# Kernel optimization log

Hardware: AMD Instinct MI355X
Metric: run time of the kernel (lower is better)

The kernel has to match this reference:

```python
import jax, jax.numpy as jnp
import numpy as np

B, D, H, W = 8, 1024, 64, 64
NH = 16
HD = D // NH
EPS = 1e-5


def _pos_encoding(n, d, dtype):
    # standard 1D sinusoidal PE over flattened spatial positions, shape (n, d)
    pos = jnp.arange(n, dtype=jnp.float32)[:, None]
    i = jnp.arange(d)[None, :]
    rates = 1.0 / (10000.0 ** ((2 * (i // 2)).astype(jnp.float32) / d))
    ang = pos * rates
    pe = jnp.where(i % 2 == 0, jnp.sin(ang), jnp.cos(ang))
    return pe.astype(dtype)


def setup_inputs() -> dict:
    key = jax.random.key(0)
    ks = jax.random.split(key, 4)
    x = jax.random.normal(ks[0], (B, D, H, W), dtype=jnp.float32)
    context_token = jax.random.normal(ks[1], (B, 1, D), dtype=jnp.float32)
    Wqkv = jax.random.normal(ks[2], (3 * D, D), dtype=jnp.float32) * 0.02
    bqkv = jnp.zeros((3 * D,), dtype=jnp.float32)
    Wo = jax.random.normal(ks[3], (D, D), dtype=jnp.float32) * 0.02
    bo = jnp.zeros((D,), dtype=jnp.float32)
    gamma = jnp.ones((D,), dtype=jnp.float32)
    beta = jnp.zeros((D,), dtype=jnp.float32)
    return {"x": x, "context_token": context_token, "Wqkv": Wqkv, "bqkv": bqkv,
            "Wo": Wo, "bo": bo, "gamma": gamma, "beta": beta}


def reference(x, context_token, Wqkv, bqkv, Wo, bo, gamma, beta):
    b, d, h, w = x.shape
    hw = h * w
    # x_flat: (B, HW, D); add positional encoding
    x_flat = x.reshape(b, d, hw).transpose(0, 2, 1)
    x_flat = x_flat + _pos_encoding(hw, d, x.dtype)[None]
    xc = jnp.concatenate([context_token, x_flat], axis=1)  # (B, S, D), S = HW+1
    s = hw + 1

    qkv = xc @ Wqkv.T + bqkv                                 # (B, S, 3D)
    q, k, v = jnp.split(qkv, 3, axis=-1)
    k = k.reshape(b, s, NH, HD)
    v = v.reshape(b, s, NH, HD)
    scale = 1.0 / jnp.sqrt(jnp.asarray(HD, x.dtype))

    # Star attention: CLS query (row 0) attends to all keys
    q0 = q[:, 0].reshape(b, NH, HD)                          # (B, NH, HD)
    scores = jnp.einsum('bhd,bshd->bhs', q0, k) * scale      # (B, NH, S)
    probs = jax.nn.softmax(scores, axis=-1)
    cls_out = jnp.einsum('bhs,bshd->bhd', probs, v).reshape(b, d)

    # Token queries attend only to the CLS key -> softmax over 1 elem = 1 -> v_cls
    v_cls = v[:, 0].reshape(b, d)                            # (B, D)
    tok_out = jnp.broadcast_to(v_cls[:, None, :], (b, hw, d))

    attn = jnp.concatenate([cls_out[:, None, :], tok_out], axis=1)  # (B, S, D)
    attn = attn @ Wo.T + bo

    res = attn + xc
    mu = jnp.mean(res, axis=-1, keepdims=True)
    var = jnp.mean((res - mu) ** 2, axis=-1, keepdims=True)
    y = (res - mu) * jax.lax.rsqrt(var + EPS) * gamma + beta

    context_token_out = y[:, 0:1, :]
    feature_map_out = y[:, 1:, :].transpose(0, 2, 1).reshape(b, d, h, w)
    return feature_map_out, context_token_out
```

## Files before the change

### kernel.cpp

```cpp
#include <hip/hip_runtime.h>
#include <math.h>

#define B_ 8
#define D_ 1024
#define HW_ 4096
#define NH_ 16
#define EPS_ 1e-5f

#define PE_OFF   0u
#define Q0_OFF   4194304u
#define VCLS_OFF 4202496u
#define UT_OFF   4210688u
#define TB_OFF   4341760u
#define SC_OFF   4349952u
#define PT_OFF   4874240u
#define P0_OFF   5398528u
#define W_OFF    5398656u
#define CLS_OFF  5529728u
#define R0_OFF   5537920u

__global__ void k_pe(float* __restrict__ pe) {
    int idx = blockIdx.x * 256 + threadIdx.x;
    int p = idx & (HW_ - 1);
    int d = idx >> 12;
    float e = (float)(2 * (d >> 1));
    float rate = exp2f(e * (-13.287712379549449f / 1024.0f));
    float ang = (float)p * rate;
    float s, c;
    sincosf(ang, &s, &c);
    pe[idx] = (d & 1) ? c : s;
}

__global__ void k_qv(const float* __restrict__ Wqkv, const float* __restrict__ bqkv,
                     const float* __restrict__ ctx,
                     float* __restrict__ q0, float* __restrict__ vcls) {
    int wid  = (blockIdx.x * 256 + threadIdx.x) >> 6;
    int lane = threadIdx.x & 63;
    int isv  = wid >> 13;
    int r    = wid & 8191;
    int b = r >> 10, i = r & 1023;
    int row = isv ? (2 * D_ + i) : i;
    const float4* wr = (const float4*)(Wqkv + (size_t)row * D_);
    const float4* cb = (const float4*)(ctx + b * D_);
    float acc = 0.0f;
    for (int k = lane; k < 256; k += 64) {
        float4 a = wr[k], c = cb[k];
        acc += a.x * c.x + a.y * c.y + a.z * c.z + a.w * c.w;
    }
    for (int o = 32; o; o >>= 1) acc += __shfl_down(acc, o);
    if (lane == 0) {
        float v = acc + bqkv[row];
        if (isv) vcls[b * D_ + i] = v; else q0[b * D_ + i] = v;
    }
}

__global__ void k_u_tb(const float* __restrict__ Wqkv,
                       const float* __restrict__ Wo, const float* __restrict__ bo,
                       const float* __restrict__ q0, const float* __restrict__ vcls,
                       float* __restrict__ u_t, float* __restrict__ t_b) {
    if (blockIdx.x < 128) {
        int b = blockIdx.x >> 4, h = blockIdx.x & 15;
        int t = threadIdx.x;
        float a0 = 0, a1 = 0, a2 = 0, a3 = 0;
        const float* q0h = q0 + b * D_ + h * 64;
        for (int j = 0; j < 64; ++j) {
            float qj = q0h[j];
            const float* wr = Wqkv + (size_t)(D_ + h * 64 + j) * D_;
            a0 += qj * wr[t];
            a1 += qj * wr[t + 256];
            a2 += qj * wr[t + 512];
            a3 += qj * wr[t + 768];
        }
        float* ub = u_t + (size_t)(b * D_) * NH_ + h;
        ub[(size_t)t * 16]          = 0.125f * a0;
        ub[(size_t)(t + 256) * 16]  = 0.125f * a1;
        ub[(size_t)(t + 512) * 16]  = 0.125f * a2;
        ub[(size_t)(t + 768) * 16]  = 0.125f * a3;
    } else {
        int wid  = (blockIdx.x - 128) * 4 + (threadIdx.x >> 6);
        int lane = threadIdx.x & 63;
        int b = wid >> 10, i = wid & 1023;
        const float4* wr = (const float4*)(Wo + (size_t)i * D_);
        const float4* vb = (const float4*)(vcls + b * D_);
        float acc = 0.0f;
        for (int k = lane; k < 256; k += 64) {
            float4 a = wr[k], c = vb[k];
            acc += a.x * c.x + a.y * c.y + a.z * c.z + a.w * c.w;
        }
        for (int o = 32; o; o >>= 1) acc += __shfl_down(acc, o);
        if (lane == 0) t_b[b * D_ + i] = acc + bo[i];
    }
}

__global__ __launch_bounds__(512) void k_main(
        const float* __restrict__ x, const float* __restrict__ pe,
        const float* __restrict__ u_t, const float* __restrict__ t_b,
        const float* __restrict__ gamma, const float* __restrict__ beta,
        float* __restrict__ scores, float* __restrict__ out) {
    int wave = threadIdx.x >> 6, lane = threadIdx.x & 63;
    int b = blockIdx.y;
    int p = blockIdx.x * 64 + lane;
    const float* xb = x + (size_t)b * D_ * HW_;
    const float* tb = t_b + b * D_;
    float acc[16];
    #pragma unroll
    for (int h = 0; h < 16; ++h) acc[h] = 0.0f;
    float sum = 0.0f, sumsq = 0.0f;
    int d0 = wave * 128;
    for (int d = d0; d < d0 + 128; ++d) {
        float xv = xb[(size_t)d * HW_ + p];
        float pv = pe[(size_t)d * HW_ + p];
        float xc = xv + pv;
        float resv = xc + tb[d];
        sum += resv;
        sumsq += resv * resv;
        const float* up = u_t + (size_t)(b * D_ + d) * 16;
        #pragma unroll
        for (int h = 0; h < 16; ++h) acc[h] += up[h] * xc;
    }
    __shared__ float red[8][18][64];
    #pragma unroll
    for (int h = 0; h < 16; ++h) red[wave][h][lane] = acc[h];
    red[wave][16][lane] = sum;
    red[wave][17][lane] = sumsq;
    __syncthreads();
    for (int id = threadIdx.x; id < 1024; id += 512) {
        int h = id >> 6, l = id & 63;
        float s = 0.0f;
        #pragma unroll
        for (int w2 = 0; w2 < 8; ++w2) s += red[w2][h][l];
        scores[(size_t)(b * 16 + h) * HW_ + blockIdx.x * 64 + l] = s;
    }
    if (threadIdx.x < 64) {
        int l = threadIdx.x;
        float S = 0.0f, SQ = 0.0f;
        #pragma unroll
        for (int w2 = 0; w2 < 8; ++w2) { S += red[w2][16][l]; SQ += red[w2][17][l]; }
        float mu = S * (1.0f / D_);
        float var = SQ * (1.0f / D_) - mu * mu;
        red[0][16][l] = mu;
        red[0][17][l] = rsqrtf(var + EPS_);
    }
    __syncthreads();
    float mu = red[0][16][lane], rstd = red[0][17][lane];
    float* ob = out + (size_t)b * D_ * HW_;
    for (int d = d0; d < d0 + 128; ++d) {
        float resv = xb[(size_t)d * HW_ + p] + pe[(size_t)d * HW_ + p] + tb[d];
        ob[(size_t)d * HW_ + p] = (resv - mu) * rstd * gamma[d] + beta[d];
    }
}

__global__ void k_softmax(const float* __restrict__ scores, const float* __restrict__ u_t,
                          const float* __restrict__ ctx,
                          float* __restrict__ probs_tok, float* __restrict__ probs0) {
    int b = blockIdx.x >> 4, h = blockIdx.x & 15;
    int t = threadIdx.x;
    __shared__ float lds[256];
    float part = 0.0f;
    for (int d = t; d < D_; d += 256)
        part += u_t[(size_t)(b * D_ + d) * 16 + h] * ctx[b * D_ + d];
    lds[t] = part; __syncthreads();
    for (int o = 128; o; o >>= 1) { if (t < o) lds[t] += lds[t + o]; __syncthreads(); }
    float s0 = lds[0];
    __syncthreads();
    const float4* sr = (const float4*)(scores + (size_t)(b * 16 + h) * HW_);
    float4 v[4];
    float m = s0;
    #pragma unroll
    for (int k = 0; k < 4; ++k) {
        v[k] = sr[t + 256 * k];
        m = fmaxf(m, fmaxf(fmaxf(v[k].x, v[k].y), fmaxf(v[k].z, v[k].w)));
    }
    lds[t] = m; __syncthreads();
    for (int o = 128; o; o >>= 1) { if (t < o) lds[t] = fmaxf(lds[t], lds[t + o]); __syncthreads(); }
    m = lds[0];
    __syncthreads();
    float zs = 0.0f;
    #pragma unroll
    for (int k = 0; k < 4; ++k) {
        v[k].x = expf(v[k].x - m); v[k].y = expf(v[k].y - m);
        v[k].z = expf(v[k].z - m); v[k].w = expf(v[k].w - m);
        zs += v[k].x + v[k].y + v[k].z + v[k].w;
    }
    float e0 = expf(s0 - m);
    lds[t] = zs; __syncthreads();
    for (int o = 128; o; o >>= 1) { if (t < o) lds[t] += lds[t + o]; __syncthreads(); }
    float inv = 1.0f / (lds[0] + e0);
    float4* pr = (float4*)(probs_tok + (size_t)(b * 16 + h) * HW_);
    #pragma unroll
    for (int k = 0; k < 4; ++k) {
        float4 o4 = v[k];
        o4.x *= inv; o4.y *= inv; o4.z *= inv; o4.w *= inv;
        pr[t + 256 * k] = o4;
    }
    if (t == 0) probs0[b * 16 + h] = e0 * inv;
}

__global__ __launch_bounds__(512) void k_wacc(
        const float* __restrict__ x, const float* __restrict__ pe,
        const float* __restrict__ probs_tok, const float* __restrict__ probs0,
        const float* __restrict__ ctx, float* __restrict__ w) {
    int wave = threadIdx.x >> 6, lane = threadIdx.x & 63;
    int b = blockIdx.y;
    int d0 = blockIdx.x * 32 + wave * 4;
    const float* xb = x + (size_t)b * D_ * HW_;
    const float* pb = probs_tok + (size_t)b * 16 * HW_;
    float acc[4][16];
    #pragma unroll
    for (int r = 0; r < 4; ++r)
        #pragma unroll
        for (int h = 0; h < 16; ++h) acc[r][h] = 0.0f;
    for (int it = 0; it < 64; ++it) {
        int p = it * 64 + lane;
        float xv[4];
        #pragma unroll
        for (int r = 0; r < 4; ++r)
            xv[r] = xb[(size_t)(d0 + r) * HW_ + p] + pe[(size_t)(d0 + r) * HW_ + p];
        #pragma unroll
        for (int h = 0; h < 16; ++h) {
            float prv = pb[(size_t)h * HW_ + p];
            #pragma unroll
            for (int r = 0; r < 4; ++r) acc[r][h] += prv * xv[r];
        }
    }
    #pragma unroll
    for (int r = 0; r < 4; ++r)
        #pragma unroll
        for (int h = 0; h < 16; ++h) {
            float v = acc[r][h];
            for (int o = 32; o; o >>= 1) v += __shfl_down(v, o);
            acc[r][h] = v;
        }
    if (lane == 0) {
        #pragma unroll
        for (int h = 0; h < 16; ++h) {
            float p0 = probs0[b * 16 + h];
            #pragma unroll
            for (int r = 0; r < 4; ++r)
                w[(size_t)(b * 16 + h) * D_ + d0 + r] = acc[r][h] + p0 * ctx[b * D_ + d0 + r];
        }
    }
}

__global__ void k_cls(const float* __restrict__ Wqkv, const float* __restrict__ bqkv,
                      const float* __restrict__ w, float* __restrict__ cls) {
    int wid  = (blockIdx.x * 256 + threadIdx.x) >> 6;
    int lane = threadIdx.x & 63;
    int b = wid >> 10, i = wid & 1023, h = i >> 6;
    const float4* wr = (const float4*)(Wqkv + (size_t)(2 * D_ + i) * D_);
    const float4* wb = (const float4*)(w + (size_t)(b * 16 + h) * D_);
    float acc = 0.0f;
    for (int k = lane; k < 256; k += 64) {
        float4 a = wr[k], c = wb[k];
        acc += a.x * c.x + a.y * c.y + a.z * c.z + a.w * c.w;
    }
    for (int o = 32; o; o >>= 1) acc += __shfl_down(acc, o);
    if (lane == 0) cls[b * D_ + i] = acc + bqkv[2 * D_ + i];
}

__global__ void k_attn0(const float* __restrict__ Wo, const float* __restrict__ bo,
                        const float* __restrict__ cls, const float* __restrict__ ctx,
                        float* __restrict__ res0) {
    int wid  = (blockIdx.x * 256 + threadIdx.x) >> 6;
    int lane = threadIdx.x & 63;
    int b = wid >> 10, i = wid & 1023;
    const float4* wr = (const float4*)(Wo + (size_t)i * D_);
    const float4* cb = (const float4*)(cls + b * D_);
    float acc = 0.0f;
    for (int k = lane; k < 256; k += 64) {
        float4 a = wr[k], c = cb[k];
        acc += a.x * c.x + a.y * c.y + a.z * c.z + a.w * c.w;
    }
    for (int o = 32; o; o >>= 1) acc += __shfl_down(acc, o);
    if (lane == 0) res0[b * D_ + i] = acc + bo[i] + ctx[b * D_ + i];
}

__global__ void k_ln0(const float* __restrict__ res0, const float* __restrict__ gamma,
                      const float* __restrict__ beta, float* __restrict__ out) {
    int b = blockIdx.x, t = threadIdx.x;
    __shared__ float lds[512];
    float v[4];
    float s = 0.0f, sq = 0.0f;
    #pragma unroll
    for (int k = 0; k < 4; ++k) {
        v[k] = res0[b * D_ + t + 256 * k];
        s += v[k]; sq += v[k] * v[k];
    }
    lds[t] = s; lds[256 + t] = sq; __syncthreads();
    for (int o = 128; o; o >>= 1) {
        if (t < o) { lds[t] += lds[t + o]; lds[256 + t] += lds[256 + t + o]; }
        __syncthreads();
    }
    float mu = lds[0] * (1.0f / D_);
    float var = lds[256] * (1.0f / D_) - mu * mu;
    float rstd = rsqrtf(var + EPS_);
    #pragma unroll
    for (int k = 0; k < 4; ++k) {
        int i = t + 256 * k;
        out[(size_t)B_ * D_ * HW_ + b * D_ + i] = (v[k] - mu) * rstd * gamma[i] + beta[i];
    }
}

extern "C" void kernel_launch(void* const* d_in, const int* in_sizes, int n_in,
                              void* d_out, int out_size, void* d_ws, size_t ws_size,
                              hipStream_t stream) {
    const float* x     = (const float*)d_in[0];
    const float* ctx   = (const float*)d_in[1];
    const float* Wqkv  = (const float*)d_in[2];
    const float* bqkv  = (const float*)d_in[3];
    const float* Wo    = (const float*)d_in[4];
    const float* bo    = (const float*)d_in[5];
    const float* gamma = (const float*)d_in[6];
    const float* beta  = (const float*)d_in[7];
    float* out = (float*)d_out;
    float* ws  = (float*)d_ws;

    float* pe    = ws + PE_OFF;
    float* q0    = ws + Q0_OFF;
    float* vcls  = ws + VCLS_OFF;
    float* u_t   = ws + UT_OFF;
    float* t_b   = ws + TB_OFF;
    float* sc    = ws + SC_OFF;
    float* pt    = ws + PT_OFF;
    float* p0    = ws + P0_OFF;
    float* w     = ws + W_OFF;
    float* cls   = ws + CLS_OFF;
    float* r0    = ws + R0_OFF;

    k_pe<<<dim3(16384), dim3(256), 0, stream>>>(pe);
    k_qv<<<dim3(4096), dim3(256), 0, stream>>>(Wqkv, bqkv, ctx, q0, vcls);
    k_u_tb<<<dim3(2176), dim3(256), 0, stream>>>(Wqkv, Wo, bo, q0, vcls, u_t, t_b);
    k_main<<<dim3(64, 8), dim3(512), 0, stream>>>(x, pe, u_t, t_b, gamma, beta, sc, out);
    k_softmax<<<dim3(128), dim3(256), 0, stream>>>(sc, u_t, ctx, pt, p0);
    k_wacc<<<dim3(32, 8), dim3(512), 0, stream>>>(x, pe, pt, p0, ctx, w);
    k_cls<<<dim3(2048), dim3(256), 0, stream>>>(Wqkv, bqkv, w, cls);
    k_attn0<<<dim3(2048), dim3(256), 0, stream>>>(Wo, bo, cls, ctx, r0);
    k_ln0<<<dim3(8), dim3(256), 0, stream>>>(r0, gamma, beta, out);
}
```

Baseline: 495.0 us.

## Fuse LayerNorm output write into weighted-accumulation pass to drop one x read

```diff
diff --git a/kernel.cpp b/kernel.cpp
--- a/kernel.cpp
+++ b/kernel.cpp
@@ -8,27 +8,29 @@
 #define EPS_ 1e-5f
 
 #define PE_OFF   0u
-#define Q0_OFF   4194304u
-#define VCLS_OFF 4202496u
-#define UT_OFF   4210688u
-#define TB_OFF   4341760u
-#define SC_OFF   4349952u
-#define PT_OFF   4874240u
-#define P0_OFF   5398528u
-#define W_OFF    5398656u
-#define CLS_OFF  5529728u
-#define R0_OFF   5537920u
+#define UT_OFF   4194304u
+#define TB_OFF   4325376u
+#define SC_OFF   4333568u
+#define Q0_OFF   4857856u
+#define VCLS_OFF 4866048u
+#define P0_OFF   4874240u
+#define MU_OFF   4874368u
+#define RS_OFF   4907136u
+#define W_OFF    4939904u
+#define CLS_OFF  5070976u
+#define R0_OFF   5079168u
 
 __global__ void k_pe(float* __restrict__ pe) {
     int idx = blockIdx.x * 256 + threadIdx.x;
-    int p = idx & (HW_ - 1);
-    int d = idx >> 12;
-    float e = (float)(2 * (d >> 1));
+    int p  = idx & (HW_ - 1);
+    int dp = idx >> 12;
+    float e = (float)(2 * dp);
     float rate = exp2f(e * (-13.287712379549449f / 1024.0f));
     float ang = (float)p * rate;
     float s, c;
     sincosf(ang, &s, &c);
-    pe[idx] = (d & 1) ? c : s;
+    pe[(size_t)(2 * dp) * HW_ + p]     = s;
+    pe[(size_t)(2 * dp + 1) * HW_ + p] = c;
 }
 
 __global__ void k_qv(const float* __restrict__ Wqkv, const float* __restrict__ bqkv,
@@ -92,61 +94,71 @@
     }
 }
 
-__global__ __launch_bounds__(512) void k_main(
+__global__ __launch_bounds__(1024) void k_scores(
         const float* __restrict__ x, const float* __restrict__ pe,
         const float* __restrict__ u_t, const float* __restrict__ t_b,
-        const float* __restrict__ gamma, const float* __restrict__ beta,
-        float* __restrict__ scores, float* __restrict__ out) {
-    int wave = threadIdx.x >> 6, lane = threadIdx.x & 63;
+        float* __restrict__ scores, float* __restrict__ mu_o, float* __restrict__ rs_o) {
+    int tid = threadIdx.x;
+    int wave = tid >> 6, lane = tid & 63;
     int b = blockIdx.y;
-    int p = blockIdx.x * 64 + lane;
-    const float* xb = x + (size_t)b * D_ * HW_;
-    const float* tb = t_b + b * D_;
-    float acc[16];
-    #pragma unroll
-    for (int h = 0; h < 16; ++h) acc[h] = 0.0f;
-    float sum = 0.0f, sumsq = 0.0f;
-    int d0 = wave * 128;
-    for (int d = d0; d < d0 + 128; ++d) {
-        float xv = xb[(size_t)d * HW_ + p];
-        float pv = pe[(size_t)d * HW_ + p];
-        float xc = xv + pv;
-        float resv = xc + tb[d];
-        sum += resv;
-        sumsq += resv * resv;
-        const float* up = u_t + (size_t)(b * D_ + d) * 16;
-        #pragma unroll
-        for (int h = 0; h < 16; ++h) acc[h] += up[h] * xc;
-    }
-    __shared__ float red[8][18][64];
-    #pragma unroll
-    for (int h = 0; h < 16; ++h) red[wave][h][lane] = acc[h];
-    red[wave][16][lane] = sum;
-    red[wave][17][lane] = sumsq;
+    int pbase = blockIdx.x * 128;
+    int p0 = pbase + lane * 2;
+    const float* xb  = x  + (size_t)b * D_ * HW_ + p0;
+    const float* peb = pe + p0;
+    const float* tb  = t_b + b * D_;
+    float acc0[16], acc1[16];
+    #pragma unroll
+    for (int h = 0; h < 16; ++h) { acc0[h] = 0.f; acc1[h] = 0.f; }
+    float s0 = 0.f, s1 = 0.f, q0s = 0.f, q1s = 0.f;
+    int dbeg = wave * 64;
+    #pragma unroll 2
+    for (int i = 0; i < 64; ++i) {
+        int d = dbeg + i;
+        float2 xv = *(const float2*)(xb  + (size_t)d * HW_);
+        float2 pv = *(const float2*)(peb + (size_t)d * HW_);
+        float xc0 = xv.x + pv.x, xc1 = xv.y + pv.y;
+        float tbd = tb[d];
+        float r0 = xc0 + tbd, r1 = xc1 + tbd;
+        s0 += r0; s1 += r1; q0s += r0 * r0; q1s += r1 * r1;
+        const float* up = u_t + ((size_t)(b * D_ + d) << 4);
+        #pragma unroll
+        for (int h = 0; h < 16; ++h) {
+            float u = up[h];
+            acc0[h] += u * xc0;
+            acc1[h] += u * xc1;
+        }
+    }
+    __shared__ float red[16][4][128];
+    #pragma unroll 1
+    for (int c = 0; c < 4; ++c) {
+        #pragma unroll
+        for (int j = 0; j < 4; ++j) {
+            red[wave][j][lane * 2]     = acc0[4 * c + j];
+            red[wave][j][lane * 2 + 1] = acc1[4 * c + j];
+        }
+        __syncthreads();
+        if (tid < 512) {
+            int hh = tid >> 7, p = tid & 127;
+            float s = 0.f;
+            #pragma unroll
+            for (int w2 = 0; w2 < 16; ++w2) s += red[w2][hh][p];
+            scores[(size_t)(b * 16 + 4 * c + hh) * HW_ + pbase + p] = s;
+        }
+        __syncthreads();
+    }
+    red[wave][0][lane * 2]     = s0;
+    red[wave][0][lane * 2 + 1] = s1;
+    red[wave][1][lane * 2]     = q0s;
+    red[wave][1][lane * 2 + 1] = q1s;
     __syncthreads();
-    for (int id = threadIdx.x; id < 1024; id += 512) {
-        int h = id >> 6, l = id & 63;
-        float s = 0.0f;
-        #pragma unroll
-        for (int w2 = 0; w2 < 8; ++w2) s += red[w2][h][l];
-        scores[(size_t)(b * 16 + h) * HW_ + blockIdx.x * 64 + l] = s;
-    }
-    if (threadIdx.x < 64) {
-        int l = threadIdx.x;
-        float S = 0.0f, SQ = 0.0f;
-        #pragma unroll
-        for (int w2 = 0; w2 < 8; ++w2) { S += red[w2][16][l]; SQ += red[w2][17][l]; }
-        float mu = S * (1.0f / D_);
-        float var = SQ * (1.0f / D_) - mu * mu;
-        red[0][16][l] = mu;
-        red[0][17][l] = rsqrtf(var + EPS_);
-    }
-    __syncthreads();
-    float mu = red[0][16][lane], rstd = red[0][17][lane];
-    float* ob = out + (size_t)b * D_ * HW_;
-    for (int d = d0; d < d0 + 128; ++d) {
-        float resv = xb[(size_t)d * HW_ + p] + pe[(size_t)d * HW_ + p] + tb[d];
-        ob[(size_t)d * HW_ + p] = (resv - mu) * rstd * gamma[d] + beta[d];
+    if (tid < 128) {
+        float S = 0.f, Q = 0.f;
+        #pragma unroll
+        for (int w2 = 0; w2 < 16; ++w2) { S += red[w2][0][tid]; Q += red[w2][1][tid]; }
+        float mu = S * (1.0f / 1024.0f);
+        float var = Q * (1.0f / 1024.0f) - mu * mu;
+        mu_o[b * HW_ + pbase + tid] = mu;
+        rs_o[b * HW_ + pbase + tid] = rsqrtf(var + EPS_);
     }
 }
 
@@ -196,31 +208,60 @@
     if (t == 0) probs0[b * 16 + h] = e0 * inv;
 }
 
-__global__ __launch_bounds__(512) void k_wacc(
+__global__ __launch_bounds__(256) void k_wacc2(
         const float* __restrict__ x, const float* __restrict__ pe,
-        const float* __restrict__ probs_tok, const float* __restrict__ probs0,
-        const float* __restrict__ ctx, float* __restrict__ w) {
+        const float* __restrict__ probs, const float* __restrict__ p0v,
+        const float* __restrict__ ctx, const float* __restrict__ t_b,
+        const float* __restrict__ mu_i, const float* __restrict__ rs_i,
+        const float* __restrict__ gamma, const float* __restrict__ beta,
+        float* __restrict__ w, float* __restrict__ out) {
     int wave = threadIdx.x >> 6, lane = threadIdx.x & 63;
     int b = blockIdx.y;
-    int d0 = blockIdx.x * 32 + wave * 4;
+    int d0 = (blockIdx.x * 4 + wave) * 4;
     const float* xb = x + (size_t)b * D_ * HW_;
-    const float* pb = probs_tok + (size_t)b * 16 * HW_;
+    const float* pb = probs + (size_t)b * 16 * HW_;
+    float* ob = out + (size_t)b * D_ * HW_;
+    float tbv[4], gv[4], bev[4];
+    #pragma unroll
+    for (int r = 0; r < 4; ++r) {
+        tbv[r] = t_b[b * D_ + d0 + r];
+        gv[r]  = gamma[d0 + r];
+        bev[r] = beta[d0 + r];
+    }
     float acc[4][16];
     #pragma unroll
     for (int r = 0; r < 4; ++r)
         #pragma unroll
-        for (int h = 0; h < 16; ++h) acc[r][h] = 0.0f;
-    for (int it = 0; it < 64; ++it) {
-        int p = it * 64 + lane;
-        float xv[4];
-        #pragma unroll
-        for (int r = 0; r < 4; ++r)
-            xv[r] = xb[(size_t)(d0 + r) * HW_ + p] + pe[(size_t)(d0 + r) * HW_ + p];
+        for (int h = 0; h < 16; ++h) acc[r][h] = 0.f;
+    #pragma unroll 1
+    for (int it = 0; it < 16; ++it) {
+        int p = it * 256 + lane * 4;
+        float4 xc4[4];
+        #pragma unroll
+        for (int r = 0; r < 4; ++r) {
+            float4 xv = *(const float4*)(xb + (size_t)(d0 + r) * HW_ + p);
+            float4 pv = *(const float4*)(pe + (size_t)(d0 + r) * HW_ + p);
+            xc4[r].x = xv.x + pv.x; xc4[r].y = xv.y + pv.y;
+            xc4[r].z = xv.z + pv.z; xc4[r].w = xv.w + pv.w;
+        }
+        float4 m4 = *(const float4*)(mu_i + b * HW_ + p);
+        float4 r4 = *(const float4*)(rs_i + b * HW_ + p);
+        #pragma unroll
+        for (int r = 0; r < 4; ++r) {
+            float4 o4;
+            o4.x = (xc4[r].x + tbv[r] - m4.x) * r4.x * gv[r] + bev[r];
+            o4.y = (xc4[r].y + tbv[r] - m4.y) * r4.y * gv[r] + bev[r];
+            o4.z = (xc4[r].z + tbv[r] - m4.z) * r4.z * gv[r] + bev[r];
+            o4.w = (xc4[r].w + tbv[r] - m4.w) * r4.w * gv[r] + bev[r];
+            *(float4*)(ob + (size_t)(d0 + r) * HW_ + p) = o4;
+        }
         #pragma unroll
         for (int h = 0; h < 16; ++h) {
-            float prv = pb[(size_t)h * HW_ + p];
+            float4 pr = *(const float4*)(pb + (size_t)h * HW_ + p);
             #pragma unroll
-            for (int r = 0; r < 4; ++r) acc[r][h] += prv * xv[r];
+            for (int r = 0; r < 4; ++r)
+                acc[r][h] += pr.x * xc4[r].x + pr.y * xc4[r].y +
+                             pr.z * xc4[r].z + pr.w * xc4[r].w;
         }
     }
     #pragma unroll
@@ -234,10 +275,10 @@
     if (lane == 0) {
         #pragma unroll
         for (int h = 0; h < 16; ++h) {
-            float p0 = probs0[b * 16 + h];
+            float pp = p0v[b * 16 + h];
             #pragma unroll
             for (int r = 0; r < 4; ++r)
-                w[(size_t)(b * 16 + h) * D_ + d0 + r] = acc[r][h] + p0 * ctx[b * D_ + d0 + r];
+                w[(size_t)(b * 16 + h) * D_ + d0 + r] = acc[r][h] + pp * ctx[b * D_ + d0 + r];
         }
     }
 }
@@ -315,24 +356,26 @@
     float* out = (float*)d_out;
     float* ws  = (float*)d_ws;
 
-    float* pe    = ws + PE_OFF;
-    float* q0    = ws + Q0_OFF;
-    float* vcls  = ws + VCLS_OFF;
-    float* u_t   = ws + UT_OFF;
-    float* t_b   = ws + TB_OFF;
-    float* sc    = ws + SC_OFF;
-    float* pt    = ws + PT_OFF;
-    float* p0    = ws + P0_OFF;
-    float* w     = ws + W_OFF;
-    float* cls   = ws + CLS_OFF;
-    float* r0    = ws + R0_OFF;
-
-    k_pe<<<dim3(16384), dim3(256), 0, stream>>>(pe);
+    float* pe   = ws + PE_OFF;
+    float* u_t  = ws + UT_OFF;
+    float* t_b  = ws + TB_OFF;
+    float* sc   = ws + SC_OFF;
+    float* q0   = ws + Q0_OFF;
+    float* vcls = ws + VCLS_OFF;
+    float* p0   = ws + P0_OFF;
+    float* mu   = ws + MU_OFF;
+    float* rs   = ws + RS_OFF;
+    float* w    = ws + W_OFF;
+    float* cls  = ws + CLS_OFF;
+    float* r0   = ws + R0_OFF;
+
+    k_pe<<<dim3(8192), dim3(256), 0, stream>>>(pe);
     k_qv<<<dim3(4096), dim3(256), 0, stream>>>(Wqkv, bqkv, ctx, q0, vcls);
     k_u_tb<<<dim3(2176), dim3(256), 0, stream>>>(Wqkv, Wo, bo, q0, vcls, u_t, t_b);
-    k_main<<<dim3(64, 8), dim3(512), 0, stream>>>(x, pe, u_t, t_b, gamma, beta, sc, out);
-    k_softmax<<<dim3(128), dim3(256), 0, stream>>>(sc, u_t, ctx, pt, p0);
-    k_wacc<<<dim3(32, 8), dim3(512), 0, stream>>>(x, pe, pt, p0, ctx, w);
+    k_scores<<<dim3(32, 8), dim3(1024), 0, stream>>>(x, pe, u_t, t_b, sc, mu, rs);
+    k_softmax<<<dim3(128), dim3(256), 0, stream>>>(sc, u_t, ctx, sc, p0);
+    k_wacc2<<<dim3(64, 8), dim3(256), 0, stream>>>(x, pe, sc, p0, ctx, t_b, mu, rs,
+                                                   gamma, beta, w, out);
     k_cls<<<dim3(2048), dim3(256), 0, stream>>>(Wqkv, bqkv, w, cls);
     k_attn0<<<dim3(2048), dim3(256), 0, stream>>>(Wo, bo, cls, ctx, r0);
     k_ln0<<<dim3(8), dim3(256), 0, stream>>>(r0, gamma, beta, out);
```

After: 429.0 us. 1.15x faster.
